# Kernel tuning notes

Hardware: AMD Instinct MI355X
Metric: run time of the kernel (lower is better)

The kernel has to match this reference:

```python
import jax, jax.numpy as jnp
import numpy as np

LN_EPS = 1e-5
L1_EPS = 1e-12  # F.normalize clamp_min eps


def _layernorm(h, g, b):
    mu = h.mean(-1, keepdims=True)
    var = ((h - mu) ** 2).mean(-1, keepdims=True)
    return (h - mu) * jax.lax.rsqrt(var + LN_EPS) * g + b


def _graph(x, wq_w, wq_b, wk_w, wk_b, gcn_w, ln_g, ln_b):
    # x: [..., n, d]
    qx = x @ wq_w.T + wq_b
    kx = x @ wk_w.T + wk_b
    dot = jnp.einsum('...nd,...md->...nm', qx, kx)
    sq = dot * dot
    adj = sq / jnp.maximum(sq.sum(-1, keepdims=True), L1_EPS)  # L1-normalized rows
    for i in range(gcn_w.shape[0]):
        h = adj @ (x @ gcn_w[i])
        x = jax.nn.relu(_layernorm(h, ln_g[i], ln_b[i]))
    return x.mean(-2)  # mean over nodes -> [..., d]


def setup_inputs() -> dict:
    key = jax.random.key(0)
    ks = jax.random.split(key, 12)
    N, FR, B, NF = 16, 32, 50, 768
    L, NC = 2, 400
    s = 1.0 / np.sqrt(NF)
    inp = {
        'feats': jax.random.normal(ks[0], (N, FR, B, NF), jnp.float32),
        'feat_global_single': jax.random.normal(ks[1], (N, NF), jnp.float32),
        'feat_single_previous': jax.random.normal(ks[2], (N, NF), jnp.float32),
        'wq_w': jax.random.normal(ks[3], (NF, NF), jnp.float32) * s,
        'wq_b': jnp.zeros((NF,), jnp.float32),
        'wk_w': jax.random.normal(ks[4], (NF, NF), jnp.float32) * s,
        'wk_b': jnp.zeros((NF,), jnp.float32),
        'gcn_w': jax.random.normal(ks[5], (L, NF, NF), jnp.float32) * s,
        'ln_g': jnp.ones((L, NF), jnp.float32),
        'ln_b': jnp.zeros((L, NF), jnp.float32),
        'fc1_w': jax.random.normal(ks[6], (NF, 2 * NF), jnp.float32) / np.sqrt(2 * NF),
        'fc1_b': jnp.zeros((NF,), jnp.float32),
        'fc2_w': jax.random.normal(ks[7], (NC, NF), jnp.float32) * s,
        'fc2_b': jnp.zeros((NC,), jnp.float32),
        't_c': 0,
    }
    return inp


def reference(feats, feat_global_single, feat_single_previous,
              wq_w, wq_b, wk_w, wk_b, gcn_w, ln_g, ln_b,
              fc1_w, fc1_b, fc2_w, fc2_b, t_c):
    N, FR, B, NF = feats.shape
    x = feats.reshape(N * FR, B, NF)
    # object-level graph (shared weights)
    x = _graph(x, wq_w, wq_b, wk_w, wk_b, gcn_w, ln_g, ln_b)  # [N*FR, NF]
    x = x.reshape(N, FR, NF)
    # frame-level graph (same shared weights)
    x = _graph(x, wq_w, wq_b, wk_w, wk_b, gcn_w, ln_g, ln_b)  # [N, NF]
    y = jnp.concatenate([x, feat_global_single], axis=-1)      # [N, 2*NF]
    # ClassifierSimple (dropout = identity in eval)
    h = jax.nn.relu(y @ fc1_w.T + fc1_b)
    logits = h @ fc2_w.T + fc2_b
    return (logits, y)
```

## Files before the change

kernel.cpp:

```cpp
#include <hip/hip_runtime.h>

typedef unsigned short u16;
typedef unsigned int   u32;
typedef __attribute__((ext_vector_type(8))) short short8;
typedef __attribute__((ext_vector_type(4))) float float4v;

__device__ __forceinline__ float bf2f(u16 u){ union{u32 i; float f;} c; c.i = ((u32)u) << 16; return c.f; }
__device__ __forceinline__ float bflo(u32 u){ union{u32 i; float f;} c; c.i = u << 16; return c.f; }
__device__ __forceinline__ float bfhi(u32 u){ union{u32 i; float f;} c; c.i = u & 0xFFFF0000u; return c.f; }
__device__ __forceinline__ u16 f2bf(float f){
  union{float f; u32 i;} c; c.f = f; u32 x = c.i;
  return (u16)((x + 0x7FFFu + ((x >> 16) & 1u)) >> 16);
}
__device__ __forceinline__ u32 pack2(float a, float b){ return (u32)f2bf(a) | ((u32)f2bf(b) << 16); }

__device__ __forceinline__ void async16(const void* g, void* l){
  __builtin_amdgcn_global_load_lds((const __attribute__((address_space(1))) void*)g,
                                   (__attribute__((address_space(3))) void*)l, 16, 0, 0);
}

__global__ void f32_to_bf16(const float* __restrict__ src, u16* __restrict__ dst, int n4)
{
  int stride = gridDim.x * 256;
  for (int i = blockIdx.x * 256 + threadIdx.x; i < n4; i += stride) {
    float4 v = ((const float4*)src)[i];
    ushort4 o; o.x = f2bf(v.x); o.y = f2bf(v.y); o.z = f2bf(v.z); o.w = f2bf(v.w);
    ((ushort4*)dst)[i] = o;
  }
}

__global__ void prep_qkw(const float* __restrict__ wq, const float* __restrict__ wk,
                         const float* __restrict__ wqb, const float* __restrict__ wkb,
                         u16* __restrict__ Wqk, float* __restrict__ biasQK)
{
  int t = blockIdx.x * 256 + threadIdx.x;
  int stride = gridDim.x * 256;
  for (int i = t; i < 294912; i += stride) {
    float4 v = (i < 147456) ? ((const float4*)wq)[i] : ((const float4*)wk)[i - 147456];
    ushort4 o; o.x = f2bf(v.x); o.y = f2bf(v.y); o.z = f2bf(v.z); o.w = f2bf(v.w);
    ((ushort4*)Wqk)[i] = o;
  }
  if (t < 768) biasQK[t] = wqb[t];
  else if (t < 1536) biasQK[t] = wkb[t - 768];
}

__global__ void prep_gcnT(const float* __restrict__ gcn, u16* __restrict__ gcnT)
{
  __shared__ float tile[32][33];
  int l = blockIdx.z;
  int d0 = blockIdx.y * 32, o0 = blockIdx.x * 32;
  int tx = threadIdx.x, ty = threadIdx.y;
  const float* src = gcn + (size_t)l * 589824;
  u16* dst = gcnT + (size_t)l * 589824;
  for (int i = 0; i < 32; i += 8) tile[ty + i][tx] = src[(size_t)(d0 + ty + i) * 768 + o0 + tx];
  __syncthreads();
  for (int i = 0; i < 32; i += 8) dst[(size_t)(o0 + ty + i) * 768 + d0 + tx] = f2bf(tile[tx][ty + i]);
}

__global__ void __launch_bounds__(256) gemm_bt(const u16* __restrict__ A, const u16* __restrict__ Bw,
                                               const float* __restrict__ bias, u16* __restrict__ C,
                                               int M, int N, int K)
{
  __shared__ __attribute__((aligned(16))) u16 As[128 * 32];
  __shared__ __attribute__((aligned(16))) u16 Bs[128 * 32];
  int tid = threadIdx.x, lane = tid & 63, wid = tid >> 6;
  int wm = wid >> 1, wn = wid & 1;
  size_t m0 = (size_t)blockIdx.x * 128, n0 = (size_t)blockIdx.y * 128;

  float4v acc[4][4];
  for (int r = 0; r < 4; r++) for (int c = 0; c < 4; c++) acc[r][c] = (float4v){0.f, 0.f, 0.f, 0.f};

  int srow = 32 * wid + (lane >> 2);
  int sq   = (lane & 3) ^ ((lane >> 3) & 3);
  const u16* gA = A  + (m0 + srow) * (size_t)K + sq * 8;
  const u16* gB = Bw + (n0 + srow) * (size_t)K + sq * 8;
  u16* lA = &As[1024 * wid];
  u16* lB = &Bs[1024 * wid];

  int l15 = lane & 15;
  int rs  = (lane >> 4) ^ ((lane >> 1) & 3);

  for (int kt = 0; kt < K; kt += 32) {
    async16(gA + kt, lA);
    async16(gA + kt + (size_t)16 * K, lA + 512);
    async16(gB + kt, lB);
    async16(gB + kt + (size_t)16 * K, lB + 512);
    __syncthreads();
    short8 af[4], bfr[4];
    for (int r = 0; r < 4; r++) af[r]  = *(const short8*)&As[(wm * 64 + r * 16 + l15) * 32 + rs * 8];
    for (int c = 0; c < 4; c++) bfr[c] = *(const short8*)&Bs[(wn * 64 + c * 16 + l15) * 32 + rs * 8];
    for (int r = 0; r < 4; r++)
      for (int c = 0; c < 4; c++)
        acc[r][c] = __builtin_amdgcn_mfma_f32_16x16x32_bf16(af[r], bfr[c], acc[r][c], 0, 0, 0);
    __syncthreads();
  }

  int quad = lane >> 4;
  for (int c = 0; c < 4; c++) {
    int n = (int)n0 + wn * 64 + c * 16 + l15;
    float bv = bias ? bias[n] : 0.f;
    for (int r = 0; r < 4; r++) {
      size_t mbase = m0 + wm * 64 + r * 16 + quad * 4;
      for (int t = 0; t < 4; t++)
        C[(mbase + t) * (size_t)N + n] = f2bf(acc[r][c][t] + bv);
    }
  }
}


template<int NP>
__global__ void __launch_bounds__(512) fused_l1(const u16* __restrict__ QK, const u16* __restrict__ H,
                                                const float* __restrict__ lng, const float* __restrict__ lnb,
                                                u16* __restrict__ adjG, u16* __restrict__ X, int n)
{
  constexpr int ST = 72;
  constexpr int SF = 66;
  constexpr int S_TPW  = (NP == 64) ? 2 : 1;
  constexpr int S2_TPW = (NP == 64) ? 2 : 1;
  __shared__ __attribute__((aligned(16))) u16 Aq[NP * 32];
  __shared__ __attribute__((aligned(16))) u16 Bk[NP * 32];
  __shared__ __attribute__((aligned(16))) float Sq[NP * SF];
  __shared__ __attribute__((aligned(16))) u16 adjb[NP * ST];
  __shared__ __attribute__((aligned(16))) u16 HT[64 * ST];
  __shared__ float rsum[NP];
  __shared__ float stats[NP][2];
  __shared__ float bc[NP][2];
  __shared__ float lg[768], lb[768];

  int g = blockIdx.x;
  int tid = threadIdx.x, lane = tid & 63, w = tid >> 6;
  int l15 = lane & 15, quad = lane >> 4;

  for (int i = tid; i < 768; i += 512) { lg[i] = lng[i]; lb[i] = lnb[i]; }
  if (tid < NP) { stats[tid][0] = 0.f; stats[tid][1] = 0.f; }

  int sidx = tid & (NP * 4 - 1);
  int srow = sidx >> 2, skq = sidx & 3;
  int wslot = skq ^ ((srow >> 1) & 3);
  bool isB = tid >= NP * 4;
  bool sact = tid < NP * 8;
  const u16* gbase = QK + ((size_t)g * n + srow) * 1536 + skq * 8 + (isB ? 768 : 0);

  int s_mt, s_nt0; bool s_act;
  if (NP == 64) { s_mt = w & 3; s_nt0 = (w >> 2) * 2; s_act = true; }
  else          { s_mt = w >> 1; s_nt0 = w & 1;       s_act = (w < 4); }

  int rslot = (lane >> 4) ^ ((lane >> 1) & 3);
  float4v sacc[S_TPW];
  for (int j = 0; j < S_TPW; j++) sacc[j] = (float4v){0.f, 0.f, 0.f, 0.f};

  for (int kt = 0; kt < 768; kt += 32) {
    uint4 v = {0, 0, 0, 0};
    if (sact && srow < n) v = *(const uint4*)(gbase + kt);
    __syncthreads();
    if (sact) ((uint4*)(isB ? Bk : Aq))[srow * 4 + wslot] = v;
    __syncthreads();
    if (s_act) {
      short8 a = *(const short8*)&Aq[(s_mt * 16 + l15) * 32 + rslot * 8];
      for (int j = 0; j < S_TPW; j++) {
        short8 b = *(const short8*)&Bk[((s_nt0 + j) * 16 + l15) * 32 + rslot * 8];
        sacc[j] = __builtin_amdgcn_mfma_f32_16x16x32_bf16(a, b, sacc[j], 0, 0, 0);
      }
    }
  }
  __syncthreads();
  if (s_act)
    for (int j = 0; j < S_TPW; j++)
      for (int t = 0; t < 4; t++) {
        int row = s_mt * 16 + quad * 4 + t, col = (s_nt0 + j) * 16 + l15;
        float v = sacc[j][t];
        Sq[row * SF + col] = v * v;
      }
  __syncthreads();
  if (tid < NP) {
    float s = 0.f;
    for (int j = 0; j < NP; j++) s += Sq[tid * SF + j];
    rsum[tid] = 1.0f / fmaxf(s, 1e-12f);
  }
  __syncthreads();
  if (tid * 8 < NP * NP) {
    int row = (tid * 8) / NP, c0 = (tid * 8) % NP;
    float rsv = rsum[row];
    u32* gadj = (u32*)(adjG + (size_t)g * NP * NP);
    for (int p = 0; p < 4; p++) {
      u32 o = pack2(Sq[row * SF + c0 + 2 * p] * rsv, Sq[row * SF + c0 + 2 * p + 1] * rsv);
      *(u32*)&adjb[row * ST + c0 + 2 * p] = o;
      gadj[(row * NP + c0) / 2 + p] = o;
    }
  }

  int m2, nt20;
  if (NP == 64) { m2 = w & 3; nt20 = (w >> 2) * 2; }
  else          { m2 = w & 1; nt20 = w >> 1; }

  float4v xacc[12][S2_TPW];
#pragma unroll
  for (int ch = 0; ch < 12; ch++) for (int j = 0; j < S2_TPW; j++) xacc[ch][j] = (float4v){0.f,0.f,0.f,0.f};

  int hj = tid >> 3, hseg = tid & 7;
#pragma unroll
  for (int ch = 0; ch < 12; ch++) {
    __syncthreads();
    if (tid < NP * 8) {
      uint4 hv = {0, 0, 0, 0};
      if (hj < n) hv = *(const uint4*)(H + ((size_t)g * n + hj) * 768 + ch * 64 + hseg * 8);
      const u16* ep = (const u16*)&hv;
      for (int i = 0; i < 8; i++) HT[(hseg * 8 + i) * ST + hj] = ep[i];
    }
    __syncthreads();
    for (int k = 0; k < NP / 32; k++) {
      short8 a = *(const short8*)&adjb[(m2 * 16 + l15) * ST + k * 32 + quad * 8];
      for (int j = 0; j < S2_TPW; j++) {
        short8 b = *(const short8*)&HT[((nt20 + j) * 16 + l15) * ST + k * 32 + quad * 8];
        xacc[ch][j] = __builtin_amdgcn_mfma_f32_16x16x32_bf16(a, b, xacc[ch][j], 0, 0, 0);
      }
    }
  }

  float ssum[4] = {0,0,0,0}, ssq[4] = {0,0,0,0};
#pragma unroll
  for (int ch = 0; ch < 12; ch++)
    for (int j = 0; j < S2_TPW; j++)
      for (int t = 0; t < 4; t++) { float v = xacc[ch][j][t]; ssum[t] += v; ssq[t] += v * v; }
  for (int m = 1; m <= 8; m <<= 1)
    for (int t = 0; t < 4; t++) { ssum[t] += __shfl_xor(ssum[t], m); ssq[t] += __shfl_xor(ssq[t], m); }
  if (l15 == 0)
    for (int t = 0; t < 4; t++) {
      atomicAdd(&stats[m2 * 16 + quad * 4 + t][0], ssum[t]);
      atomicAdd(&stats[m2 * 16 + quad * 4 + t][1], ssq[t]);
    }
  __syncthreads();
  if (tid < NP) {
    float mu = stats[tid][0] * (1.f / 768.f);
    float var = stats[tid][1] * (1.f / 768.f) - mu * mu;
    bc[tid][0] = mu; bc[tid][1] = rsqrtf(fmaxf(var, 0.f) + 1e-5f);
  }
  __syncthreads();

#pragma unroll
  for (int ch = 0; ch < 12; ch++)
    for (int j = 0; j < S2_TPW; j++)
      for (int t = 0; t < 4; t++) {
        int row = m2 * 16 + quad * 4 + t;
        if (row < n) {
          int d = ch * 64 + (nt20 + j) * 16 + l15;
          float v = fmaxf((xacc[ch][j][t] - bc[row][0]) * bc[row][1] * lg[d] + lb[d], 0.f);
          X[((size_t)g * n + row) * 768 + d] = f2bf(v);
        }
      }
}

template<int NP>
__global__ void __launch_bounds__(512) fused_l2(const u16* __restrict__ adjG, const u16* __restrict__ H,
                                                const float* __restrict__ lng, const float* __restrict__ lnb,
                                                u16* __restrict__ Xmean, int n, float inv)
{
  constexpr int ST = 72;
  constexpr int S2_TPW = (NP == 64) ? 2 : 1;
  __shared__ __attribute__((aligned(16))) u16 adjb[NP * ST];
  __shared__ __attribute__((aligned(16))) u16 HT[64 * ST];
  __shared__ float stats[NP][2];
  __shared__ float bc[NP][2];
  __shared__ float colsum[768];
  __shared__ float lg[768], lb[768];

  int g = blockIdx.x;
  int tid = threadIdx.x, lane = tid & 63, w = tid >> 6;
  int l15 = lane & 15, quad = lane >> 4;

  for (int i = tid; i < 768; i += 512) { lg[i] = lng[i]; lb[i] = lnb[i]; colsum[i] = 0.f; }
  if (tid < NP) { stats[tid][0] = 0.f; stats[tid][1] = 0.f; }
  if (tid * 8 < NP * NP) {
    int row = (tid * 8) / NP, c0 = (tid * 8) % NP;
    const u32* gadj = (const u32*)(adjG + (size_t)g * NP * NP);
    for (int p = 0; p < 4; p++)
      *(u32*)&adjb[row * ST + c0 + 2 * p] = gadj[(row * NP + c0) / 2 + p];
  }

  int m2, nt20;
  if (NP == 64) { m2 = w & 3; nt20 = (w >> 2) * 2; }
  else          { m2 = w & 1; nt20 = w >> 1; }

  float4v xacc[12][S2_TPW];
#pragma unroll
  for (int ch = 0; ch < 12; ch++) for (int j = 0; j < S2_TPW; j++) xacc[ch][j] = (float4v){0.f,0.f,0.f,0.f};

  int hj = tid >> 3, hseg = tid & 7;
#pragma unroll
  for (int ch = 0; ch < 12; ch++) {
    __syncthreads();
    if (tid < NP * 8) {
      uint4 hv = {0, 0, 0, 0};
      if (hj < n) hv = *(const uint4*)(H + ((size_t)g * n + hj) * 768 + ch * 64 + hseg * 8);
      const u16* ep = (const u16*)&hv;
      for (int i = 0; i < 8; i++) HT[(hseg * 8 + i) * ST + hj] = ep[i];
    }
    __syncthreads();
    for (int k = 0; k < NP / 32; k++) {
      short8 a = *(const short8*)&adjb[(m2 * 16 + l15) * ST + k * 32 + quad * 8];
      for (int j = 0; j < S2_TPW; j++) {
        short8 b = *(const short8*)&HT[((nt20 + j) * 16 + l15) * ST + k * 32 + quad * 8];
        xacc[ch][j] = __builtin_amdgcn_mfma_f32_16x16x32_bf16(a, b, xacc[ch][j], 0, 0, 0);
      }
    }
  }

  float ssum[4] = {0,0,0,0}, ssq[4] = {0,0,0,0};
#pragma unroll
  for (int ch = 0; ch < 12; ch++)
    for (int j = 0; j < S2_TPW; j++)
      for (int t = 0; t < 4; t++) { float v = xacc[ch][j][t]; ssum[t] += v; ssq[t] += v * v; }
  for (int m = 1; m <= 8; m <<= 1)
    for (int t = 0; t < 4; t++) { ssum[t] += __shfl_xor(ssum[t], m); ssq[t] += __shfl_xor(ssq[t], m); }
  if (l15 == 0)
    for (int t = 0; t < 4; t++) {
      atomicAdd(&stats[m2 * 16 + quad * 4 + t][0], ssum[t]);
      atomicAdd(&stats[m2 * 16 + quad * 4 + t][1], ssq[t]);
    }
  __syncthreads();
  if (tid < NP) {
    float mu = stats[tid][0] * (1.f / 768.f);
    float var = stats[tid][1] * (1.f / 768.f) - mu * mu;
    bc[tid][0] = mu; bc[tid][1] = rsqrtf(fmaxf(var, 0.f) + 1e-5f);
  }
  __syncthreads();

#pragma unroll
  for (int ch = 0; ch < 12; ch++)
    for (int j = 0; j < S2_TPW; j++)
      for (int t = 0; t < 4; t++) {
        int row = m2 * 16 + quad * 4 + t;
        int d = ch * 64 + (nt20 + j) * 16 + l15;
        float v = fmaxf((xacc[ch][j][t] - bc[row][0]) * bc[row][1] * lg[d] + lb[d], 0.f);
        float vm = (row < n) ? v : 0.f;
        vm += __shfl_xor(vm, 16);
        vm += __shfl_xor(vm, 32);
        if (quad == 0) atomicAdd(&colsum[d], vm);
      }
  __syncthreads();
  if (tid < 384)
    ((u32*)Xmean)[(size_t)g * 384 + tid] = pack2(colsum[tid * 2] * inv, colsum[tid * 2 + 1] * inv);
}

__global__ void __launch_bounds__(384) concat_y(const u16* __restrict__ Xm,
                                                const float* __restrict__ fgs, float* __restrict__ yout)
{
  int b = blockIdx.x, tid = threadIdx.x;
  u32 u = ((const u32*)Xm)[(size_t)b * 384 + tid];
  int d0 = tid * 2;
  yout[(size_t)b * 1536 + d0]     = bflo(u);
  yout[(size_t)b * 1536 + d0 + 1] = bfhi(u);
  yout[(size_t)b * 1536 + 768 + d0]     = fgs[(size_t)b * 768 + d0];
  yout[(size_t)b * 1536 + 768 + d0 + 1] = fgs[(size_t)b * 768 + d0 + 1];
}

__global__ void __launch_bounds__(256) fc1_relu(const float* __restrict__ yout,
                                                const float* __restrict__ fc1w, const float* __restrict__ fc1b,
                                                float* __restrict__ h)
{
  int o = blockIdx.x * 4 + (threadIdx.x >> 6);
  int lane = threadIdx.x & 63;
  float acc[16];
  for (int b = 0; b < 16; b++) acc[b] = 0.f;
  const float4* wr = (const float4*)(fc1w + (size_t)o * 1536);
  for (int k4 = lane; k4 < 384; k4 += 64) {
    float4 wv = wr[k4];
    for (int b = 0; b < 16; b++) {
      float4 yv = ((const float4*)(yout + (size_t)b * 1536))[k4];
      acc[b] += wv.x * yv.x + wv.y * yv.y + wv.z * yv.z + wv.w * yv.w;
    }
  }
  for (int m = 1; m <= 32; m <<= 1)
    for (int b = 0; b < 16; b++) acc[b] += __shfl_xor(acc[b], m);
  if (lane < 16) h[(size_t)lane * 768 + o] = fmaxf(acc[lane] + fc1b[o], 0.f);
}

__global__ void __launch_bounds__(256) fc2_out(const float* __restrict__ h,
                                               const float* __restrict__ fc2w, const float* __restrict__ fc2b,
                                               float* __restrict__ logits)
{
  int o = blockIdx.x * 4 + (threadIdx.x >> 6);
  int lane = threadIdx.x & 63;
  float acc[16];
  for (int b = 0; b < 16; b++) acc[b] = 0.f;
  const float4* wr = (const float4*)(fc2w + (size_t)o * 768);
  for (int k4 = lane; k4 < 192; k4 += 64) {
    float4 wv = wr[k4];
    for (int b = 0; b < 16; b++) {
      float4 hv = ((const float4*)(h + (size_t)b * 768))[k4];
      acc[b] += wv.x * hv.x + wv.y * hv.y + wv.z * hv.z + wv.w * hv.w;
    }
  }
  for (int m = 1; m <= 32; m <<= 1)
    for (int b = 0; b < 16; b++) acc[b] += __shfl_xor(acc[b], m);
  if (lane < 16) logits[(size_t)lane * 400 + o] = acc[lane] + fc2b[o];
}

extern "C" void kernel_launch(void* const* d_in, const int* in_sizes, int n_in,
                              void* d_out, int out_size, void* d_ws, size_t ws_size,
                              hipStream_t stream) {
  const float* feats = (const float*)d_in[0];
  const float* fgs   = (const float*)d_in[1];
  const float* wq_w  = (const float*)d_in[3];
  const float* wq_b  = (const float*)d_in[4];
  const float* wk_w  = (const float*)d_in[5];
  const float* wk_b  = (const float*)d_in[6];
  const float* gcn_w = (const float*)d_in[7];
  const float* ln_g  = (const float*)d_in[8];
  const float* ln_b  = (const float*)d_in[9];
  const float* fc1_w = (const float*)d_in[10];
  const float* fc1_b = (const float*)d_in[11];
  const float* fc2_w = (const float*)d_in[12];
  const float* fc2_b = (const float*)d_in[13];
  float* out  = (float*)d_out;
  float* yout = out + 16 * 400;

  char* ws = (char*)d_ws;
  size_t off = 0;
  auto alloc = [&](size_t b){ size_t r = off; off = (off + b + 255) & ~(size_t)255; return r; };
  u16*  Fb     = (u16*) (ws + alloc((size_t)25600 * 768 * 2));
  u16*  Wqk    = (u16*) (ws + alloc((size_t)1536 * 768 * 2));
  u16*  gcnT   = (u16*) (ws + alloc((size_t)2 * 768 * 768 * 2));
  float* biasQK= (float*)(ws + alloc((size_t)1536 * 4));
  u16*  Xf     = (u16*) (ws + alloc((size_t)512 * 768 * 2));
  u16*  QKf    = (u16*) (ws + alloc((size_t)512 * 1536 * 2));
  u16*  Hf     = (u16*) (ws + alloc((size_t)512 * 768 * 2));
  u16*  X1f    = (u16*) (ws + alloc((size_t)512 * 768 * 2));
  u16*  adjFb  = (u16*) (ws + alloc((size_t)16 * 32 * 32 * 2));
  u16*  Xm     = (u16*) (ws + alloc((size_t)16 * 768 * 2));
  float* hbuf  = (float*)(ws + alloc((size_t)16 * 768 * 4));
  size_t base = off;

  auto need = [&](int GC){
    size_t R = (size_t)GC * 50;
    return base + R * 1536 * 2 + 512 + R * 768 * 2 + 512 + (size_t)GC * 64 * 64 * 2 + 512;
  };
  int GC = 64;
  if (need(512) <= ws_size) GC = 512;
  else if (need(256) <= ws_size) GC = 256;
  else if (need(128) <= ws_size) GC = 128;
  int R = GC * 50;
  size_t off2 = base;
  auto alloc2 = [&](size_t b){ size_t r = off2; off2 = (off2 + b + 255) & ~(size_t)255; return r; };
  u16* QKc  = (u16*)(ws + alloc2((size_t)R * 1536 * 2));
  u16* Hc   = (u16*)(ws + alloc2((size_t)R * 768 * 2));
  u16* adjGc= (u16*)(ws + alloc2((size_t)GC * 64 * 64 * 2));
  u16* X1c  = QKc;
  u16* H2c  = Hc;

  f32_to_bf16<<<4800, 256, 0, stream>>>(feats, Fb, 25600 * 768 / 4);
  prep_qkw<<<288, 256, 0, stream>>>(wq_w, wk_w, wq_b, wk_b, Wqk, biasQK);
  prep_gcnT<<<dim3(24, 24, 2), dim3(32, 8), 0, stream>>>(gcn_w, gcnT);

  int nchunks = 512 / GC;
  for (int c = 0; c < nchunks; c++) {
    const u16* fc = Fb + (size_t)c * GC * 50 * 768;
    gemm_bt<<<dim3(R / 128, 12), 256, 0, stream>>>(fc, Wqk, biasQK, QKc, R, 1536, 768);
    gemm_bt<<<dim3(R / 128, 6), 256, 0, stream>>>(fc, gcnT, nullptr, Hc, R, 768, 768);
    fused_l1<64><<<GC, 512, 0, stream>>>(QKc, Hc, ln_g, ln_b, adjGc, X1c, 50);
    gemm_bt<<<dim3(R / 128, 6), 256, 0, stream>>>(X1c, gcnT + (size_t)768 * 768, nullptr, H2c, R, 768, 768);
    fused_l2<64><<<GC, 512, 0, stream>>>(adjGc, H2c, ln_g + 768, ln_b + 768,
                                         Xf + (size_t)c * GC * 768, 50, 1.f / 50.f);
  }

  gemm_bt<<<dim3(4, 12), 256, 0, stream>>>(Xf, Wqk, biasQK, QKf, 512, 1536, 768);
  gemm_bt<<<dim3(4, 6), 256, 0, stream>>>(Xf, gcnT, nullptr, Hf, 512, 768, 768);
  fused_l1<32><<<16, 512, 0, stream>>>(QKf, Hf, ln_g, ln_b, adjFb, X1f, 32);
  gemm_bt<<<dim3(4, 6), 256, 0, stream>>>(X1f, gcnT + (size_t)768 * 768, nullptr, Hf, 512, 768, 768);
  fused_l2<32><<<16, 512, 0, stream>>>(adjFb, Hf, ln_g + 768, ln_b + 768, Xm, 32, 1.f / 32.f);

  concat_y<<<16, 384, 0, stream>>>(Xm, fgs, yout);
  fc1_relu<<<192, 256, 0, stream>>>(yout, fc1_w, fc1_b, hbuf);
  fc2_out<<<100, 256, 0, stream>>>(hbuf, fc2_w, fc2_b, out);
}
```

Measured before the change: 586.2 us.

## Fuse feats bf16 conversion into GEMM and merge Q/K/H projections

```diff
diff --git a/kernel.cpp b/kernel.cpp
--- a/kernel.cpp
+++ b/kernel.cpp
@@ -19,45 +19,37 @@
                                    (__attribute__((address_space(3))) void*)l, 16, 0, 0);
 }
 
-__global__ void f32_to_bf16(const float* __restrict__ src, u16* __restrict__ dst, int n4)
-{
-  int stride = gridDim.x * 256;
-  for (int i = blockIdx.x * 256 + threadIdx.x; i < n4; i += stride) {
-    float4 v = ((const float4*)src)[i];
-    ushort4 o; o.x = f2bf(v.x); o.y = f2bf(v.y); o.z = f2bf(v.z); o.w = f2bf(v.w);
-    ((ushort4*)dst)[i] = o;
-  }
-}
-
 __global__ void prep_qkw(const float* __restrict__ wq, const float* __restrict__ wk,
                          const float* __restrict__ wqb, const float* __restrict__ wkb,
-                         u16* __restrict__ Wqk, float* __restrict__ biasQK)
+                         u16* __restrict__ QHB, float* __restrict__ biasQH)
 {
   int t = blockIdx.x * 256 + threadIdx.x;
   int stride = gridDim.x * 256;
   for (int i = t; i < 294912; i += stride) {
     float4 v = (i < 147456) ? ((const float4*)wq)[i] : ((const float4*)wk)[i - 147456];
     ushort4 o; o.x = f2bf(v.x); o.y = f2bf(v.y); o.z = f2bf(v.z); o.w = f2bf(v.w);
-    ((ushort4*)Wqk)[i] = o;
-  }
-  if (t < 768) biasQK[t] = wqb[t];
-  else if (t < 1536) biasQK[t] = wkb[t - 768];
-}
-
-__global__ void prep_gcnT(const float* __restrict__ gcn, u16* __restrict__ gcnT)
+    ((ushort4*)QHB)[i] = o;
+  }
+  if (t < 768) biasQH[t] = wqb[t];
+  else if (t < 1536) biasQH[t] = wkb[t - 768];
+  else if (t < 2304) biasQH[t] = 0.f;
+}
+
+__global__ void prep_gcnT(const float* __restrict__ gcn, u16* __restrict__ QHB, u16* __restrict__ gcnT1)
 {
   __shared__ float tile[32][33];
   int l = blockIdx.z;
   int d0 = blockIdx.y * 32, o0 = blockIdx.x * 32;
   int tx = threadIdx.x, ty = threadIdx.y;
   const float* src = gcn + (size_t)l * 589824;
-  u16* dst = gcnT + (size_t)l * 589824;
+  u16* dst = (l == 0) ? (QHB + (size_t)1536 * 768) : gcnT1;
   for (int i = 0; i < 32; i += 8) tile[ty + i][tx] = src[(size_t)(d0 + ty + i) * 768 + o0 + tx];
   __syncthreads();
   for (int i = 0; i < 32; i += 8) dst[(size_t)(o0 + ty + i) * 768 + d0 + tx] = f2bf(tile[tx][ty + i]);
 }
 
-__global__ void __launch_bounds__(256) gemm_bt(const u16* __restrict__ A, const u16* __restrict__ Bw,
+template<bool AF32>
+__global__ void __launch_bounds__(256) gemm_bt(const void* __restrict__ Aptr, const u16* __restrict__ Bw,
                                                const float* __restrict__ bias, u16* __restrict__ C,
                                                int M, int N, int K)
 {
@@ -72,19 +64,35 @@
 
   int srow = 32 * wid + (lane >> 2);
   int sq   = (lane & 3) ^ ((lane >> 3) & 3);
-  const u16* gA = A  + (m0 + srow) * (size_t)K + sq * 8;
-  const u16* gB = Bw + (n0 + srow) * (size_t)K + sq * 8;
+  const u16*  gB  = Bw + (n0 + srow) * (size_t)K + sq * 8;
+  u16* lB = &Bs[1024 * wid];
+  const float* gAf0 = AF32 ? ((const float*)Aptr + (m0 + srow) * (size_t)K + sq * 8) : nullptr;
+  const float* gAf1 = AF32 ? ((const float*)Aptr + (m0 + srow + 16) * (size_t)K + sq * 8) : nullptr;
+  const u16*  gA16 = AF32 ? nullptr : ((const u16*)Aptr + (m0 + srow) * (size_t)K + sq * 8);
   u16* lA = &As[1024 * wid];
-  u16* lB = &Bs[1024 * wid];
+  int wslot16 = srow * 32 + (lane & 3) * 8;
 
   int l15 = lane & 15;
   int rs  = (lane >> 4) ^ ((lane >> 1) & 3);
 
   for (int kt = 0; kt < K; kt += 32) {
-    async16(gA + kt, lA);
-    async16(gA + kt + (size_t)16 * K, lA + 512);
-    async16(gB + kt, lB);
-    async16(gB + kt + (size_t)16 * K, lB + 512);
+    if (AF32) {
+      float4 f0 = *(const float4*)(gAf0 + kt);
+      float4 f1 = *(const float4*)(gAf0 + kt + 4);
+      float4 f2 = *(const float4*)(gAf1 + kt);
+      float4 f3 = *(const float4*)(gAf1 + kt + 4);
+      async16(gB + kt, lB);
+      async16(gB + kt + (size_t)16 * K, lB + 512);
+      uint4 o0 = { pack2(f0.x,f0.y), pack2(f0.z,f0.w), pack2(f1.x,f1.y), pack2(f1.z,f1.w) };
+      uint4 o1 = { pack2(f2.x,f2.y), pack2(f2.z,f2.w), pack2(f3.x,f3.y), pack2(f3.z,f3.w) };
+      *(uint4*)&As[wslot16]            = o0;
+      *(uint4*)&As[wslot16 + 16 * 32]  = o1;
+    } else {
+      async16(gA16 + kt, lA);
+      async16(gA16 + kt + (size_t)16 * K, lA + 512);
+      async16(gB + kt, lB);
+      async16(gB + kt + (size_t)16 * K, lB + 512);
+    }
     __syncthreads();
     short8 af[4], bfr[4];
     for (int r = 0; r < 4; r++) af[r]  = *(const short8*)&As[(wm * 64 + r * 16 + l15) * 32 + rs * 8];
@@ -109,17 +117,12 @@
 
 
 template<int NP>
-__global__ void __launch_bounds__(512) fused_l1(const u16* __restrict__ QK, const u16* __restrict__ H,
+__global__ void __launch_bounds__(512) fused_l1(const u16* __restrict__ QH,
                                                 const float* __restrict__ lng, const float* __restrict__ lnb,
                                                 u16* __restrict__ adjG, u16* __restrict__ X, int n)
 {
   constexpr int ST = 72;
-  constexpr int SF = 66;
-  constexpr int S_TPW  = (NP == 64) ? 2 : 1;
-  constexpr int S2_TPW = (NP == 64) ? 2 : 1;
-  __shared__ __attribute__((aligned(16))) u16 Aq[NP * 32];
-  __shared__ __attribute__((aligned(16))) u16 Bk[NP * 32];
-  __shared__ __attribute__((aligned(16))) float Sq[NP * SF];
+  constexpr int TPW = (NP == 64) ? 2 : 1;
   __shared__ __attribute__((aligned(16))) u16 adjb[NP * ST];
   __shared__ __attribute__((aligned(16))) u16 HT[64 * ST];
   __shared__ float rsum[NP];
@@ -132,85 +135,83 @@
   int l15 = lane & 15, quad = lane >> 4;
 
   for (int i = tid; i < 768; i += 512) { lg[i] = lng[i]; lb[i] = lnb[i]; }
-  if (tid < NP) { stats[tid][0] = 0.f; stats[tid][1] = 0.f; }
-
-  int sidx = tid & (NP * 4 - 1);
-  int srow = sidx >> 2, skq = sidx & 3;
-  int wslot = skq ^ ((srow >> 1) & 3);
-  bool isB = tid >= NP * 4;
-  bool sact = tid < NP * 8;
-  const u16* gbase = QK + ((size_t)g * n + srow) * 1536 + skq * 8 + (isB ? 768 : 0);
-
-  int s_mt, s_nt0; bool s_act;
-  if (NP == 64) { s_mt = w & 3; s_nt0 = (w >> 2) * 2; s_act = true; }
-  else          { s_mt = w >> 1; s_nt0 = w & 1;       s_act = (w < 4); }
-
-  int rslot = (lane >> 4) ^ ((lane >> 1) & 3);
-  float4v sacc[S_TPW];
-  for (int j = 0; j < S_TPW; j++) sacc[j] = (float4v){0.f, 0.f, 0.f, 0.f};
-
-  for (int kt = 0; kt < 768; kt += 32) {
-    uint4 v = {0, 0, 0, 0};
-    if (sact && srow < n) v = *(const uint4*)(gbase + kt);
-    __syncthreads();
-    if (sact) ((uint4*)(isB ? Bk : Aq))[srow * 4 + wslot] = v;
-    __syncthreads();
-    if (s_act) {
-      short8 a = *(const short8*)&Aq[(s_mt * 16 + l15) * 32 + rslot * 8];
-      for (int j = 0; j < S_TPW; j++) {
-        short8 b = *(const short8*)&Bk[((s_nt0 + j) * 16 + l15) * 32 + rslot * 8];
-        sacc[j] = __builtin_amdgcn_mfma_f32_16x16x32_bf16(a, b, sacc[j], 0, 0, 0);
+  if (tid < NP) { rsum[tid] = 0.f; stats[tid][0] = 0.f; stats[tid][1] = 0.f; }
+  __syncthreads();
+
+  int mt, nt0; bool s_act;
+  if (NP == 64) { mt = w & 3; nt0 = (w >> 2) * 2; s_act = true; }
+  else          { mt = w & 1; nt0 = w >> 1;       s_act = (w < 4); }
+
+  int rowA = mt * 16 + l15;
+  bool aok = rowA < n;
+  const u16* pA  = QH + ((size_t)g * n + rowA) * 2304 + quad * 8;
+  int rowB0 = (nt0) * 16 + l15, rowB1 = (nt0 + TPW - 1) * 16 + l15;
+  bool b0ok = rowB0 < n, b1ok = rowB1 < n;
+  const u16* pB0 = QH + ((size_t)g * n + rowB0) * 2304 + 768 + quad * 8;
+  const u16* pB1 = QH + ((size_t)g * n + rowB1) * 2304 + 768 + quad * 8;
+
+  float4v sacc[TPW];
+  for (int j = 0; j < TPW; j++) sacc[j] = (float4v){0.f, 0.f, 0.f, 0.f};
+
+  if (s_act) {
+    for (int kt = 0; kt < 768; kt += 32) {
+      uint4 av = {0,0,0,0}, bv0 = {0,0,0,0}, bv1 = {0,0,0,0};
+      if (aok)  av  = *(const uint4*)(pA + kt);
+      if (b0ok) bv0 = *(const uint4*)(pB0 + kt);
+      if (TPW == 2 && b1ok) bv1 = *(const uint4*)(pB1 + kt);
+      short8 a = *(short8*)&av;
+      sacc[0] = __builtin_amdgcn_mfma_f32_16x16x32_bf16(a, *(short8*)&bv0, sacc[0], 0, 0, 0);
+      if (TPW == 2)
+        sacc[1] = __builtin_amdgcn_mfma_f32_16x16x32_bf16(a, *(short8*)&bv1, sacc[1], 0, 0, 0);
+    }
+    for (int t = 0; t < 4; t++) {
+      float s = 0.f;
+      for (int j = 0; j < TPW; j++) { float v = sacc[j][t]; s += v * v; }
+      s += __shfl_xor(s, 1); s += __shfl_xor(s, 2); s += __shfl_xor(s, 4); s += __shfl_xor(s, 8);
+      if (l15 == 0) atomicAdd(&rsum[mt * 16 + quad * 4 + t], s);
+    }
+  }
+  __syncthreads();
+  if (tid < NP) rsum[tid] = 1.0f / fmaxf(rsum[tid], 1e-12f);
+  __syncthreads();
+  if (s_act) {
+    u16* gadj = adjG + (size_t)g * NP * NP;
+    for (int j = 0; j < TPW; j++)
+      for (int t = 0; t < 4; t++) {
+        int row = mt * 16 + quad * 4 + t, col = (nt0 + j) * 16 + l15;
+        float v = sacc[j][t];
+        u16 b = f2bf(v * v * rsum[row]);
+        adjb[row * ST + col] = b;
+        gadj[row * NP + col] = b;
       }
-    }
-  }
-  __syncthreads();
-  if (s_act)
-    for (int j = 0; j < S_TPW; j++)
-      for (int t = 0; t < 4; t++) {
-        int row = s_mt * 16 + quad * 4 + t, col = (s_nt0 + j) * 16 + l15;
-        float v = sacc[j][t];
-        Sq[row * SF + col] = v * v;
-      }
-  __syncthreads();
-  if (tid < NP) {
-    float s = 0.f;
-    for (int j = 0; j < NP; j++) s += Sq[tid * SF + j];
-    rsum[tid] = 1.0f / fmaxf(s, 1e-12f);
-  }
-  __syncthreads();
-  if (tid * 8 < NP * NP) {
-    int row = (tid * 8) / NP, c0 = (tid * 8) % NP;
-    float rsv = rsum[row];
-    u32* gadj = (u32*)(adjG + (size_t)g * NP * NP);
-    for (int p = 0; p < 4; p++) {
-      u32 o = pack2(Sq[row * SF + c0 + 2 * p] * rsv, Sq[row * SF + c0 + 2 * p + 1] * rsv);
-      *(u32*)&adjb[row * ST + c0 + 2 * p] = o;
-      gadj[(row * NP + c0) / 2 + p] = o;
-    }
-  }
+  }
+  __syncthreads();
 
   int m2, nt20;
   if (NP == 64) { m2 = w & 3; nt20 = (w >> 2) * 2; }
   else          { m2 = w & 1; nt20 = w >> 1; }
 
-  float4v xacc[12][S2_TPW];
-#pragma unroll
-  for (int ch = 0; ch < 12; ch++) for (int j = 0; j < S2_TPW; j++) xacc[ch][j] = (float4v){0.f,0.f,0.f,0.f};
-
-  int hj = tid >> 3, hseg = tid & 7;
+  float4v xacc[12][TPW];
+#pragma unroll
+  for (int ch = 0; ch < 12; ch++) for (int j = 0; j < TPW; j++) xacc[ch][j] = (float4v){0.f,0.f,0.f,0.f};
+
+  int hj  = tid & (NP - 1);
+  int hseg= (NP == 64) ? w : ((tid >> 5) & 7);
+  bool hact = (NP == 64) ? true : (tid < NP * 8);
+
 #pragma unroll
   for (int ch = 0; ch < 12; ch++) {
-    __syncthreads();
-    if (tid < NP * 8) {
-      uint4 hv = {0, 0, 0, 0};
-      if (hj < n) hv = *(const uint4*)(H + ((size_t)g * n + hj) * 768 + ch * 64 + hseg * 8);
+    uint4 hv = {0,0,0,0};
+    if (hact && hj < n) hv = *(const uint4*)(QH + ((size_t)g * n + hj) * 2304 + 1536 + ch * 64 + hseg * 8);
+    __syncthreads();
+    if (hact) {
       const u16* ep = (const u16*)&hv;
       for (int i = 0; i < 8; i++) HT[(hseg * 8 + i) * ST + hj] = ep[i];
     }
     __syncthreads();
     for (int k = 0; k < NP / 32; k++) {
       short8 a = *(const short8*)&adjb[(m2 * 16 + l15) * ST + k * 32 + quad * 8];
-      for (int j = 0; j < S2_TPW; j++) {
+      for (int j = 0; j < TPW; j++) {
         short8 b = *(const short8*)&HT[((nt20 + j) * 16 + l15) * ST + k * 32 + quad * 8];
         xacc[ch][j] = __builtin_amdgcn_mfma_f32_16x16x32_bf16(a, b, xacc[ch][j], 0, 0, 0);
       }
@@ -220,7 +221,7 @@
   float ssum[4] = {0,0,0,0}, ssq[4] = {0,0,0,0};
 #pragma unroll
   for (int ch = 0; ch < 12; ch++)
-    for (int j = 0; j < S2_TPW; j++)
+    for (int j = 0; j < TPW; j++)
       for (int t = 0; t < 4; t++) { float v = xacc[ch][j][t]; ssum[t] += v; ssq[t] += v * v; }
   for (int m = 1; m <= 8; m <<= 1)
     for (int t = 0; t < 4; t++) { ssum[t] += __shfl_xor(ssum[t], m); ssq[t] += __shfl_xor(ssq[t], m); }
@@ -239,7 +240,7 @@
 
 #pragma unroll
   for (int ch = 0; ch < 12; ch++)
-    for (int j = 0; j < S2_TPW; j++)
+    for (int j = 0; j < TPW; j++)
       for (int t = 0; t < 4; t++) {
         int row = m2 * 16 + quad * 4 + t;
         if (row < n) {
@@ -256,7 +257,7 @@
                                                 u16* __restrict__ Xmean, int n, float inv)
 {
   constexpr int ST = 72;
-  constexpr int S2_TPW = (NP == 64) ? 2 : 1;
+  constexpr int TPW = (NP == 64) ? 2 : 1;
   __shared__ __attribute__((aligned(16))) u16 adjb[NP * ST];
   __shared__ __attribute__((aligned(16))) u16 HT[64 * ST];
   __shared__ float stats[NP][2];
@@ -272,33 +273,35 @@
   if (tid < NP) { stats[tid][0] = 0.f; stats[tid][1] = 0.f; }
   if (tid * 8 < NP * NP) {
     int row = (tid * 8) / NP, c0 = (tid * 8) % NP;
-    const u32* gadj = (const u32*)(adjG + (size_t)g * NP * NP);
-    for (int p = 0; p < 4; p++)
-      *(u32*)&adjb[row * ST + c0 + 2 * p] = gadj[(row * NP + c0) / 2 + p];
+    uint4 v = *(const uint4*)(adjG + (size_t)g * NP * NP + row * NP + c0);
+    *(uint4*)&adjb[row * ST + c0] = v;
   }
 
   int m2, nt20;
   if (NP == 64) { m2 = w & 3; nt20 = (w >> 2) * 2; }
   else          { m2 = w & 1; nt20 = w >> 1; }
 
-  float4v xacc[12][S2_TPW];
-#pragma unroll
-  for (int ch = 0; ch < 12; ch++) for (int j = 0; j < S2_TPW; j++) xacc[ch][j] = (float4v){0.f,0.f,0.f,0.f};
-
-  int hj = tid >> 3, hseg = tid & 7;
+  float4v xacc[12][TPW];
+#pragma unroll
+  for (int ch = 0; ch < 12; ch++) for (int j = 0; j < TPW; j++) xacc[ch][j] = (float4v){0.f,0.f,0.f,0.f};
+
+  int hj  = tid & (NP - 1);
+  int hseg= (NP == 64) ? w : ((tid >> 5) & 7);
+  bool hact = (NP == 64) ? true : (tid < NP * 8);
+
 #pragma unroll
   for (int ch = 0; ch < 12; ch++) {
-    __syncthreads();
-    if (tid < NP * 8) {
-      uint4 hv = {0, 0, 0, 0};
-      if (hj < n) hv = *(const uint4*)(H + ((size_t)g * n + hj) * 768 + ch * 64 + hseg * 8);
+    uint4 hv = {0,0,0,0};
+    if (hact && hj < n) hv = *(const uint4*)(H + ((size_t)g * n + hj) * 768 + ch * 64 + hseg * 8);
+    __syncthreads();
+    if (hact) {
       const u16* ep = (const u16*)&hv;
       for (int i = 0; i < 8; i++) HT[(hseg * 8 + i) * ST + hj] = ep[i];
     }
     __syncthreads();
     for (int k = 0; k < NP / 32; k++) {
       short8 a = *(const short8*)&adjb[(m2 * 16 + l15) * ST + k * 32 + quad * 8];
-      for (int j = 0; j < S2_TPW; j++) {
+      for (int j = 0; j < TPW; j++) {
         short8 b = *(const short8*)&HT[((nt20 + j) * 16 + l15) * ST + k * 32 + quad * 8];
         xacc[ch][j] = __builtin_amdgcn_mfma_f32_16x16x32_bf16(a, b, xacc[ch][j], 0, 0, 0);
       }
@@ -308,7 +311,7 @@
   float ssum[4] = {0,0,0,0}, ssq[4] = {0,0,0,0};
 #pragma unroll
   for (int ch = 0; ch < 12; ch++)
-    for (int j = 0; j < S2_TPW; j++)
+    for (int j = 0; j < TPW; j++)
       for (int t = 0; t < 4; t++) { float v = xacc[ch][j][t]; ssum[t] += v; ssq[t] += v * v; }
   for (int m = 1; m <= 8; m <<= 1)
     for (int t = 0; t < 4; t++) { ssum[t] += __shfl_xor(ssum[t], m); ssq[t] += __shfl_xor(ssq[t], m); }
@@ -327,7 +330,7 @@
 
 #pragma unroll
   for (int ch = 0; ch < 12; ch++)
-    for (int j = 0; j < S2_TPW; j++)
+    for (int j = 0; j < TPW; j++)
       for (int t = 0; t < 4; t++) {
         int row = m2 * 16 + quad * 4 + t;
         int d = ch * 64 + (nt20 + j) * 16 + l15;
@@ -418,14 +421,13 @@
   char* ws = (char*)d_ws;
   size_t off = 0;
   auto alloc = [&](size_t b){ size_t r = off; off = (off + b + 255) & ~(size_t)255; return r; };
-  u16*  Fb     = (u16*) (ws + alloc((size_t)25600 * 768 * 2));
-  u16*  Wqk    = (u16*) (ws + alloc((size_t)1536 * 768 * 2));
-  u16*  gcnT   = (u16*) (ws + alloc((size_t)2 * 768 * 768 * 2));
-  float* biasQK= (float*)(ws + alloc((size_t)1536 * 4));
+  u16*  QHB    = (u16*) (ws + alloc((size_t)2304 * 768 * 2));
+  u16*  gcnT1  = (u16*) (ws + alloc((size_t)768 * 768 * 2));
+  float* biasQH= (float*)(ws + alloc((size_t)2304 * 4));
   u16*  Xf     = (u16*) (ws + alloc((size_t)512 * 768 * 2));
-  u16*  QKf    = (u16*) (ws + alloc((size_t)512 * 1536 * 2));
-  u16*  Hf     = (u16*) (ws + alloc((size_t)512 * 768 * 2));
+  u16*  QHf    = (u16*) (ws + alloc((size_t)512 * 2304 * 2));
   u16*  X1f    = (u16*) (ws + alloc((size_t)512 * 768 * 2));
+  u16*  H2f    = (u16*) (ws + alloc((size_t)512 * 768 * 2));
   u16*  adjFb  = (u16*) (ws + alloc((size_t)16 * 32 * 32 * 2));
   u16*  Xm     = (u16*) (ws + alloc((size_t)16 * 768 * 2));
   float* hbuf  = (float*)(ws + alloc((size_t)16 * 768 * 4));
@@ -433,7 +435,7 @@
 
   auto need = [&](int GC){
     size_t R = (size_t)GC * 50;
-    return base + R * 1536 * 2 + 512 + R * 768 * 2 + 512 + (size_t)GC * 64 * 64 * 2 + 512;
+    return base + R * 2304 * 2 + 512 + R * 768 * 2 + 512 + (size_t)GC * 64 * 64 * 2 + 512;
   };
   int GC = 64;
   if (need(512) <= ws_size) GC = 512;
@@ -442,32 +444,28 @@
   int R = GC * 50;
   size_t off2 = base;
   auto alloc2 = [&](size_t b){ size_t r = off2; off2 = (off2 + b + 255) & ~(size_t)255; return r; };
-  u16* QKc  = (u16*)(ws + alloc2((size_t)R * 1536 * 2));
-  u16* Hc   = (u16*)(ws + alloc2((size_t)R * 768 * 2));
-  u16* adjGc= (u16*)(ws + alloc2((size_t)GC * 64 * 64 * 2));
-  u16* X1c  = QKc;
-  u16* H2c  = Hc;
-
-  f32_to_bf16<<<4800, 256, 0, stream>>>(feats, Fb, 25600 * 768 / 4);
-  prep_qkw<<<288, 256, 0, stream>>>(wq_w, wk_w, wq_b, wk_b, Wqk, biasQK);
-  prep_gcnT<<<dim3(24, 24, 2), dim3(32, 8), 0, stream>>>(gcn_w, gcnT);
+  u16* QHc   = (u16*)(ws + alloc2((size_t)R * 2304 * 2));
+  u16* X1c   = (u16*)(ws + alloc2((size_t)R * 768 * 2));
+  u16* adjGc = (u16*)(ws + alloc2((size_t)GC * 64 * 64 * 2));
+  u16* H2c   = QHc;
+
+  prep_qkw<<<288, 256, 0, stream>>>(wq_w, wk_w, wq_b, wk_b, QHB, biasQH);
+  prep_gcnT<<<dim3(24, 24, 2), dim3(32, 8), 0, stream>>>(gcn_w, QHB, gcnT1);
 
   int nchunks = 512 / GC;
   for (int c = 0; c < nchunks; c++) {
-    const u16* fc = Fb + (size_t)c * GC * 50 * 768;
-    gemm_bt<<<dim3(R / 128, 12), 256, 0, stream>>>(fc, Wqk, biasQK, QKc, R, 1536, 768);
-    gemm_bt<<<dim3(R / 128, 6), 256, 0, stream>>>(fc, gcnT, nullptr, Hc, R, 768, 768);
-    fused_l1<64><<<GC, 512, 0, stream>>>(QKc, Hc, ln_g, ln_b, adjGc, X1c, 50);
-    gemm_bt<<<dim3(R / 128, 6), 256, 0, stream>>>(X1c, gcnT + (size_t)768 * 768, nullptr, H2c, R, 768, 768);
+    const float* fc = feats + (size_t)c * GC * 50 * 768;
+    gemm_bt<true><<<dim3(R / 128, 18), 256, 0, stream>>>(fc, QHB, biasQH, QHc, R, 2304, 768);
+    fused_l1<64><<<GC, 512, 0, stream>>>(QHc, ln_g, ln_b, adjGc, X1c, 50);
+    gemm_bt<false><<<dim3(R / 128, 6), 256, 0, stream>>>(X1c, gcnT1, nullptr, H2c, R, 768, 768);
     fused_l2<64><<<GC, 512, 0, stream>>>(adjGc, H2c, ln_g + 768, ln_b + 768,
                                          Xf + (size_t)c * GC * 768, 50, 1.f / 50.f);
   }
 
-  gemm_bt<<<dim3(4, 12), 256, 0, stream>>>(Xf, Wqk, biasQK, QKf, 512, 1536, 768);
-  gemm_bt<<<dim3(4, 6), 256, 0, stream>>>(Xf, gcnT, nullptr, Hf, 512, 768, 768);
-  fused_l1<32><<<16, 512, 0, stream>>>(QKf, Hf, ln_g, ln_b, adjFb, X1f, 32);
-  gemm_bt<<<dim3(4, 6), 256, 0, stream>>>(X1f, gcnT + (size_t)768 * 768, nullptr, Hf, 512, 768, 768);
-  fused_l2<32><<<16, 512, 0, stream>>>(adjFb, Hf, ln_g + 768, ln_b + 768, Xm, 32, 1.f / 32.f);
+  gemm_bt<false><<<dim3(4, 18), 256, 0, stream>>>(Xf, QHB, biasQH, QHf, 512, 2304, 768);
+  fused_l1<32><<<16, 512, 0, stream>>>(QHf, ln_g, ln_b, adjFb, X1f, 32);
+  gemm_bt<false><<<dim3(4, 6), 256, 0, stream>>>(X1f, gcnT1, nullptr, H2f, 512, 768, 768);
+  fused_l2<32><<<16, 512, 0, stream>>>(adjFb, H2f, ln_g + 768, ln_b + 768, Xm, 32, 1.f / 32.f);
 
   concat_y<<<16, 384, 0, stream>>>(Xm, fgs, yout);
   fc1_relu<<<192, 256, 0, stream>>>(yout, fc1_w, fc1_b, hbuf);
```

Result: faster. 570.6 us (-2.7%).
